# Performance work log

Hardware: AMD Instinct MI355X
Metric: run time of the kernel (lower is better)

The kernel has to match this reference:

```python
import jax, jax.numpy as jnp
import numpy as np

N_NODES = 100000
N_EDGES = 1250000
N_GRAPHS = 256
IN_DIM, HID, OUT = 7, 64, 2


def setup_inputs() -> dict:
    key = jax.random.key(0)
    ks = jax.random.split(key, 10)
    x = jax.random.normal(ks[0], (N_NODES, IN_DIM), dtype=jnp.float32)
    edge_index = jax.random.randint(ks[1], (2, N_EDGES), 0, N_NODES, dtype=jnp.int64)
    batch = jnp.sort(jax.random.randint(ks[2], (N_NODES,), 0, N_GRAPHS, dtype=jnp.int64))
    def glorot(k, shape):
        lim = float(np.sqrt(6.0 / (shape[0] + shape[1])))
        return jax.random.uniform(k, shape, jnp.float32, -lim, lim)
    return {
        "x": x, "edge_index": edge_index, "batch": batch,
        "W1": glorot(ks[3], (IN_DIM, HID)), "b1": jnp.zeros((HID,), jnp.float32),
        "W2": glorot(ks[4], (HID, HID)),   "b2": jnp.zeros((HID,), jnp.float32),
        "W3": glorot(ks[5], (HID, HID)),   "b3": jnp.zeros((HID,), jnp.float32),
        "Wl": glorot(ks[6], (HID, OUT)),   "bl": jnp.zeros((OUT,), jnp.float32),
    }


def _gcn_conv(x, src, dst, W, b, n_nodes):
    # PyG GCNConv: add self-loops, symmetric deg^{-1/2} normalization,
    # linear transform, scatter-add aggregation at target nodes, + bias.
    deg = jax.ops.segment_sum(jnp.ones_like(dst, dtype=x.dtype), dst, num_segments=n_nodes)
    dinv = jnp.where(deg > 0, jax.lax.rsqrt(deg), 0.0)
    norm = dinv[src] * dinv[dst]                      # [E+N]
    h = x @ W                                         # [N, out]
    msg = h[src] * norm[:, None]                      # gather + scale
    out = jax.ops.segment_sum(msg, dst, num_segments=n_nodes)
    return out + b


def reference(x, edge_index, batch, W1, b1, W2, b2, W3, b3, Wl, bl):
    n = x.shape[0]
    loop = jnp.arange(n, dtype=edge_index.dtype)
    src = jnp.concatenate([edge_index[0], loop])      # self-loops appended once
    dst = jnp.concatenate([edge_index[1], loop])

    h = jax.nn.relu(_gcn_conv(x, src, dst, W1, b1, n))
    h = jax.nn.relu(_gcn_conv(h, src, dst, W2, b2, n))
    h = _gcn_conv(h, src, dst, W3, b3, n)

    # global_mean_pool over graphs
    sums = jax.ops.segment_sum(h, batch, num_segments=N_GRAPHS)
    cnt = jax.ops.segment_sum(jnp.ones((n,), h.dtype), batch, num_segments=N_GRAPHS)
    pooled = sums / jnp.maximum(cnt, 1.0)[:, None]    # [G, HID]

    # dropout is identity in eval mode
    return pooled @ Wl + bl                           # [G, 2]
```

## Files before the change

### kernel.cpp

```cpp
#include <hip/hip_runtime.h>
#include <hip/hip_fp16.h>

#define HID 64
#define NGRAPHS 256
#define CHUNK 4096
#define BKTSZ 512
#define BKTSH 9
#define PSH 17
#define PMASK 0x1FFFF

typedef _Float16 half8 __attribute__((ext_vector_type(8)));
typedef float f32x4 __attribute__((ext_vector_type(4)));



__global__ __launch_bounds__(256) void k_hist(
        const int* __restrict__ dst, const float* __restrict__ W2,
        const float* __restrict__ W3, const float* __restrict__ Wl,
        __half* __restrict__ Wf2, float* __restrict__ W3l,
        int* __restrict__ H, float* __restrict__ gsum,
        int e, int nbkt, int nchunk) {
    __shared__ int cnt4[4][256];
    const int t = threadIdx.x, b = blockIdx.x;
    const int gtid = b * 256 + t;
    if (gtid < 512) {
        int p = gtid;
        int kt = p >> 8, c = (p >> 6) & 3, lane = p & 63;
        int quad = lane >> 4, m = lane & 15;
#pragma unroll
        for (int j = 0; j < 8; ++j) {
            int k = kt * 32 + quad * 8 + j;
            int ch = c * 16 + m;
            Wf2[(size_t)p * 8 + j] = __float2half(W2[k * HID + ch]);
        }
    }
    if (b == 0) {
        for (int i = t; i < NGRAPHS * 2; i += 256) gsum[i] = 0.0f;
        if (t < 128) {
            int j = t >> 1, o = t & 1;
            float s = 0.0f;
#pragma unroll
            for (int k = 0; k < HID; ++k) s += W3[j * HID + k] * Wl[k * 2 + o];
            W3l[j * 2 + o] = s;
        }
    }
    for (int i = t; i < 1024; i += 256) ((int*)cnt4)[i] = 0;
    __syncthreads();
    const int w = t >> 6;
#pragma unroll
    for (int it = 0; it < CHUNK / 1024; ++it) {
        int idx = b * CHUNK + it * 1024 + t * 4;
        if (idx + 3 < e) {
            int4 d = *(const int4*)(dst + idx);
            atomicAdd(&cnt4[w][d.x >> BKTSH], 1);
            atomicAdd(&cnt4[w][d.y >> BKTSH], 1);
            atomicAdd(&cnt4[w][d.z >> BKTSH], 1);
            atomicAdd(&cnt4[w][d.w >> BKTSH], 1);
        } else {
            for (int i = idx; i < e && i < idx + 4; ++i)
                atomicAdd(&cnt4[w][dst[i] >> BKTSH], 1);
        }
    }
    __syncthreads();
    for (int i = t; i < nbkt; i += 256)
        H[i * nchunk + b] = cnt4[0][i] + cnt4[1][i] + cnt4[2][i] + cnt4[3][i];
}


__global__ __launch_bounds__(256) void k_scan(const int* __restrict__ in,
                                              int* __restrict__ outp,
                                              int* __restrict__ bsum, int n) {
    __shared__ int sh[256];
    const int t = threadIdx.x;
    const int base = blockIdx.x * 1024 + t * 4;
    int v[4];
    int s = 0;
#pragma unroll
    for (int k = 0; k < 4; k++) {
        int i = base + k;
        v[k] = (i < n) ? in[i] : 0;
        s += v[k];
    }
    sh[t] = s;
    __syncthreads();
#pragma unroll
    for (int off = 1; off < 256; off <<= 1) {
        int add = (t >= off) ? sh[t - off] : 0;
        __syncthreads();
        sh[t] += add;
        __syncthreads();
    }
    int run = sh[t] - s;
#pragma unroll
    for (int k = 0; k < 4; k++) {
        int i = base + k;
        if (i < n) outp[i] = run;
        run += v[k];
    }
    if (t == 255) bsum[blockIdx.x] = sh[255];
}


__global__ __launch_bounds__(256) void k_scatter(
        const int* __restrict__ src, const int* __restrict__ dst,
        const int* __restrict__ Hs, const int* __restrict__ bsum,
        int* __restrict__ packed, int e, int nbkt, int nchunk, int nscan) {
    __shared__ int off[256];
    __shared__ int lc[256];
    __shared__ int bscan[64];
    const int t = threadIdx.x, b = blockIdx.x;
    if (t < 64) bscan[t] = (t < nscan) ? bsum[t] : 0;
    __syncthreads();
#pragma unroll
    for (int o = 1; o < 64; o <<= 1) {
        int add = (t < 64 && t >= o) ? bscan[t - o] : 0;
        __syncthreads();
        if (t < 64) bscan[t] += add;
        __syncthreads();
    }
    for (int i = t; i < nbkt; i += 256) {
        int idx = i * nchunk + b;
        int q = idx >> 10;
        off[i] = Hs[idx] + (q ? bscan[q - 1] : 0);
        lc[i] = 0;
    }
    __syncthreads();
#pragma unroll
    for (int it = 0; it < CHUNK / 1024; ++it) {
        int idx = b * CHUNK + it * 1024 + t * 4;
        if (idx + 3 < e) {
            int4 d = *(const int4*)(dst + idx);
            int4 s = *(const int4*)(src + idx);
            int b0 = d.x >> BKTSH, b1 = d.y >> BKTSH;
            int b2 = d.z >> BKTSH, b3 = d.w >> BKTSH;
            int r0 = atomicAdd(&lc[b0], 1);
            int r1 = atomicAdd(&lc[b1], 1);
            int r2 = atomicAdd(&lc[b2], 1);
            int r3 = atomicAdd(&lc[b3], 1);
            packed[off[b0] + r0] = s.x | ((d.x & (BKTSZ - 1)) << PSH);
            packed[off[b1] + r1] = s.y | ((d.y & (BKTSZ - 1)) << PSH);
            packed[off[b2] + r2] = s.z | ((d.z & (BKTSZ - 1)) << PSH);
            packed[off[b3] + r3] = s.w | ((d.w & (BKTSZ - 1)) << PSH);
        } else {
            for (int i = idx; i < e && i < idx + 4; ++i) {
                int dd = dst[i];
                int bk = dd >> BKTSH;
                int r = atomicAdd(&lc[bk], 1);
                packed[off[bk] + r] = src[i] | ((dd & (BKTSZ - 1)) << PSH);
            }
        }
    }
}


__global__ __launch_bounds__(256) void k_csr_build(
        const int* __restrict__ packed, const int* __restrict__ Hs,
        const int* __restrict__ bsum, int* __restrict__ rowptr,
        float* __restrict__ dinv, int* __restrict__ csr,
        const float* __restrict__ x, float* __restrict__ xt,
        int e, int n, int nbkt, int nchunk, int nscan) {
    __shared__ int cnt[BKTSZ];
    __shared__ int pref[BKTSZ];
    __shared__ int ssum[256];
    __shared__ int cnt2[BKTSZ];
    __shared__ int bscan[64];
    const int t = threadIdx.x, bkt = blockIdx.x;
    if (t < 64) bscan[t] = (t < nscan) ? bsum[t] : 0;
    if (bkt == 0 && t == 0) rowptr[n] = e;
    cnt[t] = 0; cnt[t + 256] = 0;
    cnt2[t] = 0; cnt2[t + 256] = 0;
    __syncthreads();
#pragma unroll
    for (int o = 1; o < 64; o <<= 1) {
        int add = (t < 64 && t >= o) ? bscan[t - o] : 0;
        __syncthreads();
        if (t < 64) bscan[t] += add;
        __syncthreads();
    }
    int i0 = bkt * nchunk;
    int q0 = i0 >> 10;
    int segStart = Hs[i0] + (q0 ? bscan[q0 - 1] : 0);
    int segEnd = e;
    if (bkt + 1 < nbkt) {
        int i1 = (bkt + 1) * nchunk;
        int q1 = i1 >> 10;
        segEnd = Hs[i1] + (q1 ? bscan[q1 - 1] : 0);
    }
    for (int j = segStart + t; j < segEnd; j += 256)
        atomicAdd(&cnt[(packed[j] >> PSH) & (BKTSZ - 1)], 1);
    __syncthreads();
    int a0 = cnt[2 * t], a1 = cnt[2 * t + 1];
    int s = a0 + a1;
    ssum[t] = s;
    __syncthreads();
#pragma unroll
    for (int off = 1; off < 256; off <<= 1) {
        int add = (t >= off) ? ssum[t - off] : 0;
        __syncthreads();
        ssum[t] += add;
        __syncthreads();
    }
    int p = ssum[t] - s;
    pref[2 * t] = p;
    pref[2 * t + 1] = p + a0;
    __syncthreads();
    for (int i = t; i < BKTSZ; i += 256) {
        int node = bkt * BKTSZ + i;
        if (node < n) {
            rowptr[node] = segStart + pref[i];
            dinv[node] = rsqrtf((float)(cnt[i] + 1));
        }
    }
    for (int j = segStart + t; j < segEnd; j += 256) {
        int pk = packed[j];
        int ld = (pk >> PSH) & (BKTSZ - 1);
        int r = atomicAdd(&cnt2[ld], 1);
        csr[segStart + pref[ld] + r] = pk & PMASK;
    }
    for (int i = t; i < BKTSZ * 8; i += 256) {
        int nl = i >> 3, k = i & 7;
        int node = bkt * BKTSZ + nl;
        if (node < n)
            xt[(size_t)node * 8 + k] =
                (k < 7) ? x[(size_t)node * 7 + k] * rsqrtf((float)(cnt[nl] + 1))
                        : 0.0f;
    }
}

__device__ __forceinline__ void add_h8(float* a, int4 raw) {
    const __half2* p = (const __half2*)&raw;
#pragma unroll
    for (int i = 0; i < 4; ++i) {
        float2 f = __half22float2(p[i]);
        a[2 * i] += f.x;
        a[2 * i + 1] += f.y;
    }
}


__global__ __launch_bounds__(256) void k_aggx_gemm(
        const int* __restrict__ rowptr, const int* __restrict__ csr,
        const float* __restrict__ xt, const float* __restrict__ b,
        const float* __restrict__ dinv, const float* __restrict__ W1,
        const __half* __restrict__ Wf, __half* __restrict__ hout,
        int n_nodes) {
    __shared__ __half act[16 * 72];
    __shared__ float W1s[7 * HID];
    const int t = threadIdx.x;
    const int n0 = blockIdx.x * 16;
    const int nl = t >> 4;
    const int node = n0 + nl;
    const int l16 = t & 15;
    const float4* xt4 = (const float4*)xt;
    const float4* b4 = (const float4*)b;

    for (int i = t; i < 7 * HID; i += 256) W1s[i] = W1[i];

    float acc8[8];
#pragma unroll
    for (int i = 0; i < 8; ++i) acc8[i] = 0.0f;

    float4 av = make_float4(0.0f, 0.0f, 0.0f, 0.0f);
    float dv = 0.0f;
    if (node < n_nodes) {
        int beg = rowptr[node], end = rowptr[node + 1];
        dv = dinv[node];
        if (l16 == 0) {
            float4 s0 = xt4[(size_t)node * 2];
            float4 s1 = xt4[(size_t)node * 2 + 1];
            acc8[0] += s0.x; acc8[1] += s0.y; acc8[2] += s0.z; acc8[3] += s0.w;
            acc8[4] += s1.x; acc8[5] += s1.y; acc8[6] += s1.z; acc8[7] += s1.w;
        }
        int j = beg;
        for (; j + 15 < end; j += 16) {
            int e = csr[j + l16];
            float4 r0 = xt4[(size_t)e * 2];
            float4 r1 = xt4[(size_t)e * 2 + 1];
            acc8[0] += r0.x; acc8[1] += r0.y; acc8[2] += r0.z; acc8[3] += r0.w;
            acc8[4] += r1.x; acc8[5] += r1.y; acc8[6] += r1.z; acc8[7] += r1.w;
        }
        int rem = end - j;
        if (l16 < rem) {
            int e = csr[j + l16];
            float4 r0 = xt4[(size_t)e * 2];
            float4 r1 = xt4[(size_t)e * 2 + 1];
            acc8[0] += r0.x; acc8[1] += r0.y; acc8[2] += r0.z; acc8[3] += r0.w;
            acc8[4] += r1.x; acc8[5] += r1.y; acc8[6] += r1.z; acc8[7] += r1.w;
        }
    }
#pragma unroll
    for (int o = 8; o; o >>= 1)
#pragma unroll
        for (int i = 0; i < 7; ++i)
            acc8[i] += __shfl_xor(acc8[i], o, 16);

    if (node < n_nodes) {
        float4 bb = b4[l16];
#pragma unroll
        for (int i = 0; i < 4; ++i) {
            int c = l16 * 4 + i;
            float dot = 0.0f;
#pragma unroll
            for (int k = 0; k < 7; ++k) dot += acc8[k] * W1s[k * HID + c];
            float v = ((const float*)&bb)[i] + dv * dot;
            ((float*)&av)[i] = fmaxf(v, 0.0f);
        }
    }
    {
        __half2 p0 = __floats2half2_rn(av.x, av.y);
        __half2 p1 = __floats2half2_rn(av.z, av.w);
        int2 pk;
        pk.x = *(int*)&p0;
        pk.y = *(int*)&p1;
        *(int2*)&act[nl * 72 + l16 * 4] = pk;
    }
    __syncthreads();

    const int wave = t >> 6, lane = t & 63;
    const int quad = lane >> 4, m = lane & 15;
    const half8* Wf8 = (const half8*)Wf;
    f32x4 acc = {0.0f, 0.0f, 0.0f, 0.0f};
#pragma unroll
    for (int kt = 0; kt < 2; ++kt) {
        half8 a = *(const half8*)&act[m * 72 + kt * 32 + quad * 8];
        half8 bv = Wf8[(kt * 4 + wave) * 64 + lane];
        acc = __builtin_amdgcn_mfma_f32_16x16x32_f16(a, bv, acc, 0, 0, 0);
    }
#pragma unroll
    for (int r = 0; r < 4; ++r) {
        int nd = n0 + quad * 4 + r;
        if (nd < n_nodes)
            hout[(size_t)nd * HID + wave * 16 + m] =
                __float2half(acc[r] * dinv[nd]);
    }
}


__global__ __launch_bounds__(256) void k_agg_z(
        const int* __restrict__ rowptr, const int* __restrict__ csr,
        const __half* __restrict__ h, const float* __restrict__ b,
        const float* __restrict__ dinv, const float* __restrict__ W3l,
        float2* __restrict__ zbuf, int n_nodes) {
    const int t = threadIdx.x;
    const int n0 = blockIdx.x * 16;
    const int nl = t >> 4;
    const int node = n0 + nl;
    const int l16 = t & 15;
    const int cb = l16 & 7;
    const int hf = l16 >> 3;
    const int4* h16 = (const int4*)h;

    float w3l0[8], w3l1[8], bb8[8];
#pragma unroll
    for (int i = 0; i < 8; ++i) {
        w3l0[i] = W3l[(cb * 8 + i) * 2 + 0];
        w3l1[i] = W3l[(cb * 8 + i) * 2 + 1];
        bb8[i] = b[cb * 8 + i];
    }

    float acc8[8];
#pragma unroll
    for (int i = 0; i < 8; ++i) acc8[i] = 0.0f;

    float dv = 0.0f;
    if (node < n_nodes) {
        int beg = rowptr[node], end = rowptr[node + 1];
        dv = dinv[node];
        if (hf == 0)
            add_h8(acc8, h16[(size_t)node * 8 + cb]);
        int j = beg;
        for (; j + 7 < end; j += 8) {
            int e8 = csr[j + (l16 & 7)];
            int4 r[4];
#pragma unroll
            for (int q = 0; q < 4; ++q) {
                int sid = __shfl(e8, 2 * q + hf, 8);
                r[q] = h16[(size_t)sid * 8 + cb];
            }
#pragma unroll
            for (int q = 0; q < 4; ++q) add_h8(acc8, r[q]);
        }
        if (j + 3 < end) {
            int e4 = csr[j + (l16 & 3)];
            int4 r[2];
#pragma unroll
            for (int q = 0; q < 2; ++q) {
                int sid = __shfl(e4, 2 * q + hf, 4);
                r[q] = h16[(size_t)sid * 8 + cb];
            }
            add_h8(acc8, r[0]);
            add_h8(acc8, r[1]);
            j += 4;
        }
        for (; j < end; ++j)
            if (hf == 0) add_h8(acc8, h16[(size_t)csr[j] * 8 + cb]);
    }
#pragma unroll
    for (int i = 0; i < 8; ++i) acc8[i] += __shfl_xor(acc8[i], 8, 16);
    float p0 = 0.0f, p1 = 0.0f;
#pragma unroll
    for (int i = 0; i < 8; ++i) {
        float v = fmaxf(bb8[i] + dv * acc8[i], 0.0f);
        p0 += v * w3l0[i];
        p1 += v * w3l1[i];
    }
#pragma unroll
    for (int o = 4; o; o >>= 1) {
        p0 += __shfl_xor(p0, o, 16);
        p1 += __shfl_xor(p1, o, 16);
    }
    if (node < n_nodes && l16 == 0)
        zbuf[node] = make_float2(p0 * dv, p1 * dv);
}


__global__ __launch_bounds__(256) void k_zagg_part(
        const int* __restrict__ rowptr, const int* __restrict__ csr,
        const float2* __restrict__ zbuf, const float* __restrict__ dinv,
        const int* __restrict__ batch, float* __restrict__ partv,
        int* __restrict__ partg, float* __restrict__ gsum, int n_nodes) {
    __shared__ float2 ys[16];
    __shared__ int bg[16];
    const int t = threadIdx.x;
    const int n0 = blockIdx.x * 16;
    const int nl = t >> 4;
    const int node = n0 + nl;
    const int q = t & 15;

    if (t < 16) {
        int nd = n0 + t;
        bg[t] = (nd < n_nodes) ? batch[nd] : -1;
    }

    float2 yv = make_float2(0.0f, 0.0f);
    if (node < n_nodes) {
        int beg = rowptr[node], end = rowptr[node + 1];
        float2 acc = make_float2(0.0f, 0.0f);
        if (q == 0) acc = zbuf[node];
        int j = beg;
        for (; j + 15 < end; j += 16) {
            int e = csr[j + q];
            float2 v = zbuf[e];
            acc.x += v.x; acc.y += v.y;
        }
        int rem = end - j;
        if (q < rem) {
            int e = csr[j + q];
            float2 v = zbuf[e];
            acc.x += v.x; acc.y += v.y;
        }
#pragma unroll
        for (int o = 8; o; o >>= 1) {
            acc.x += __shfl_xor(acc.x, o, 16);
            acc.y += __shfl_xor(acc.y, o, 16);
        }
        float dv = dinv[node];
        yv = make_float2(acc.x * dv, acc.y * dv);
    }
    if (q == 0) ys[nl] = yv;
    __syncthreads();

    if (t == 0) {
        const int g0 = bg[0];
        const int g15 = bg[15];
        float2 s0 = make_float2(0.0f, 0.0f), s1 = make_float2(0.0f, 0.0f);
        for (int i = 0; i < 16; ++i) {
            int g = bg[i];
            float2 v = ys[i];
            if (g == g0) { s0.x += v.x; s0.y += v.y; }
            else if (g == g15) { s1.x += v.x; s1.y += v.y; }
            else if (g >= 0) {
                atomicAdd(&gsum[g * 2 + 0], v.x);
                atomicAdd(&gsum[g * 2 + 1], v.y);
            }
        }
        partv[(size_t)blockIdx.x * 4 + 0] = s0.x;
        partv[(size_t)blockIdx.x * 4 + 1] = s0.y;
        partv[(size_t)blockIdx.x * 4 + 2] = s1.x;
        partv[(size_t)blockIdx.x * 4 + 3] = s1.y;
        partg[blockIdx.x * 2 + 0] = g0;
        partg[blockIdx.x * 2 + 1] = (g15 != g0) ? g15 : -1;
    }
}


__global__ __launch_bounds__(256) void k_pool_head(
        const float* __restrict__ partv, const int* __restrict__ partg,
        const float* __restrict__ gsum, const int* __restrict__ batch,
        const float* __restrict__ b3, const float* __restrict__ Wl,
        const float* __restrict__ bl, float* __restrict__ out, int n_nodes) {
    int g = blockIdx.x;
    int lo = 0, hi = n_nodes;
    while (lo < hi) { int m = (lo + hi) >> 1; if (batch[m] < g) lo = m + 1; else hi = m; }
    int nstart = lo;
    hi = n_nodes;
    while (lo < hi) { int m = (lo + hi) >> 1; if (batch[m] < g + 1) lo = m + 1; else hi = m; }
    int nend = lo;

    const int t = threadIdx.x;
    float ax = 0.0f, ay = 0.0f;
    if (nend > nstart) {
        int b0 = nstart >> 4, b1 = (nend - 1) >> 4;
        for (int b = b0 + t; b <= b1; b += 256) {
            if (partg[b * 2 + 0] == g) { ax += partv[(size_t)b * 4 + 0]; ay += partv[(size_t)b * 4 + 1]; }
            if (partg[b * 2 + 1] == g) { ax += partv[(size_t)b * 4 + 2]; ay += partv[(size_t)b * 4 + 3]; }
        }
    }
    __shared__ float rx[256], ry[256];
    rx[t] = ax; ry[t] = ay;
    __syncthreads();
    for (int s2 = 128; s2; s2 >>= 1) {
        if (t < s2) { rx[t] += rx[t + s2]; ry[t] += ry[t + s2]; }
        __syncthreads();
    }
    if (t < 2) {
        float cntf = fmaxf((float)(nend - nstart), 1.0f);
        float s = ((t == 0) ? rx[0] : ry[0]) + gsum[g * 2 + t];
        float hb = 0.0f;
        for (int c = 0; c < HID; ++c) hb += b3[c] * Wl[c * 2 + t];
        out[g * 2 + t] = s / cntf + hb + bl[t];
    }
}


extern "C" void kernel_launch(void* const* d_in, const int* in_sizes, int n_in,
                              void* d_out, int out_size, void* d_ws, size_t ws_size,
                              hipStream_t stream) {
    const float* x     = (const float*)d_in[0];
    const int*   ei    = (const int*)d_in[1];
    const int*   batch = (const int*)d_in[2];
    const float* W1    = (const float*)d_in[3];
    const float* b1    = (const float*)d_in[4];
    const float* W2    = (const float*)d_in[5];
    const float* b2    = (const float*)d_in[6];
    const float* W3    = (const float*)d_in[7];
    const float* b3    = (const float*)d_in[8];
    const float* Wl    = (const float*)d_in[9];
    const float* bl    = (const float*)d_in[10];
    float* out = (float*)d_out;

    const int N = in_sizes[0] / 7;
    const int E = in_sizes[1] / 2;
    const int* src = ei;
    const int* dst = ei + E;

    const int nbkt   = (N + BKTSZ - 1) >> BKTSH;
    const int nchunk = (E + CHUNK - 1) / CHUNK;
    const int lenH   = nbkt * nchunk;
    const int nscan  = (lenH + 1023) / 1024;

    char* ws = (char*)d_ws;
    size_t off = 0;
    auto carve = [&](size_t bytes) {
        void* p = ws + off;
        off = (off + bytes + 255) & ~(size_t)255;
        return p;
    };
    int*    H      = (int*)carve((size_t)lenH * 4);
    int*    Hs     = (int*)carve((size_t)lenH * 4);
    int*    bsum   = (int*)carve(512 * 4);
    int*    packed = (int*)carve((size_t)E * 4);
    int*    csr    = (int*)carve((size_t)E * 4);
    int*    rowptr = (int*)carve((size_t)(N + 1) * 4);
    float*  dinv   = (float*)carve((size_t)N * 4);
    __half* Wf2    = (__half*)carve(4096 * 2);
    float*  W3l    = (float*)carve(128 * 4);
    float*  gsum   = (float*)carve((size_t)NGRAPHS * 2 * 4);
    float*  xt     = (float*)carve((size_t)(N + 64) * 8 * 4);
    __half* bufB   = (__half*)carve((size_t)(N + 64) * HID * 2);
    float2* zbuf   = (float2*)carve((size_t)(N + 64) * 8);

    const int nb_agg = (N + 15) / 16;
    float* partv = (float*)carve((size_t)nb_agg * 4 * 4);
    int*   partg = (int*)carve((size_t)nb_agg * 2 * 4);

    k_hist<<<nchunk, 256, 0, stream>>>(dst, W2, W3, Wl, Wf2, W3l, H, gsum,
                                       E, nbkt, nchunk);
    k_scan<<<nscan, 256, 0, stream>>>(H, Hs, bsum, lenH);
    k_scatter<<<nchunk, 256, 0, stream>>>(src, dst, Hs, bsum, packed,
                                          E, nbkt, nchunk, nscan);
    k_csr_build<<<nbkt, 256, 0, stream>>>(packed, Hs, bsum, rowptr, dinv, csr,
                                          x, xt, E, N, nbkt, nchunk, nscan);

    k_aggx_gemm<<<nb_agg, 256, 0, stream>>>(rowptr, csr, xt, b1, dinv, W1,
                                            Wf2, bufB, N);
    k_agg_z<<<nb_agg, 256, 0, stream>>>(rowptr, csr, bufB, b2, dinv, W3l,
                                        zbuf, N);
    k_zagg_part<<<nb_agg, 256, 0, stream>>>(rowptr, csr, zbuf, dinv, batch,
                                            partv, partg, gsum, N);

    k_pool_head<<<NGRAPHS, 256, 0, stream>>>(partv, partg, gsum, batch,
                                             b3, Wl, bl, out, N);
}
```

Before: 195.2 us.

## Replace two-pass bucket sort CSR build with global atomic degree count and scatter

Replaces the bucketed histogram, scan, packed scatter and per-bucket CSR build with a direct per-node degree count using global atomics, a per-block scan that also computes dinv and pre-scaled features, and a scatter that places each edge using a global atomic cursor per destination. This removes the packed intermediate buffer, one pass over the edges and one kernel launch. In exchange it relies on heavily contended global atomics on random addresses and gives a nondeterministic neighbor order within each row, which can change floating-point summation order and locality in later aggregation.

```diff
diff --git a/kernel.cpp b/kernel.cpp
--- a/kernel.cpp
+++ b/kernel.cpp
@@ -3,24 +3,17 @@
 
 #define HID 64
 #define NGRAPHS 256
-#define CHUNK 4096
-#define BKTSZ 512
-#define BKTSH 9
-#define PSH 17
-#define PMASK 0x1FFFF
 
 typedef _Float16 half8 __attribute__((ext_vector_type(8)));
 typedef float f32x4 __attribute__((ext_vector_type(4)));
 
 
 
-__global__ __launch_bounds__(256) void k_hist(
+__global__ __launch_bounds__(256) void k_deg(
         const int* __restrict__ dst, const float* __restrict__ W2,
         const float* __restrict__ W3, const float* __restrict__ Wl,
         __half* __restrict__ Wf2, float* __restrict__ W3l,
-        int* __restrict__ H, float* __restrict__ gsum,
-        int e, int nbkt, int nchunk) {
-    __shared__ int cnt4[4][256];
+        int* __restrict__ deg, float* __restrict__ gsum, int e) {
     const int t = threadIdx.x, b = blockIdx.x;
     const int gtid = b * 256 + t;
     if (gtid < 512) {
@@ -44,186 +37,112 @@
             W3l[j * 2 + o] = s;
         }
     }
-    for (int i = t; i < 1024; i += 256) ((int*)cnt4)[i] = 0;
-    __syncthreads();
-    const int w = t >> 6;
-#pragma unroll
-    for (int it = 0; it < CHUNK / 1024; ++it) {
-        int idx = b * CHUNK + it * 1024 + t * 4;
-        if (idx + 3 < e) {
-            int4 d = *(const int4*)(dst + idx);
-            atomicAdd(&cnt4[w][d.x >> BKTSH], 1);
-            atomicAdd(&cnt4[w][d.y >> BKTSH], 1);
-            atomicAdd(&cnt4[w][d.z >> BKTSH], 1);
-            atomicAdd(&cnt4[w][d.w >> BKTSH], 1);
-        } else {
-            for (int i = idx; i < e && i < idx + 4; ++i)
-                atomicAdd(&cnt4[w][dst[i] >> BKTSH], 1);
-        }
-    }
-    __syncthreads();
-    for (int i = t; i < nbkt; i += 256)
-        H[i * nchunk + b] = cnt4[0][i] + cnt4[1][i] + cnt4[2][i] + cnt4[3][i];
-}
-
-
-__global__ __launch_bounds__(256) void k_scan(const int* __restrict__ in,
-                                              int* __restrict__ outp,
-                                              int* __restrict__ bsum, int n) {
+    int idx = b * 1024 + t * 4;
+    if (idx + 3 < e) {
+        int4 d = *(const int4*)(dst + idx);
+        atomicAdd(&deg[d.x], 1);
+        atomicAdd(&deg[d.y], 1);
+        atomicAdd(&deg[d.z], 1);
+        atomicAdd(&deg[d.w], 1);
+    } else {
+        for (int i = idx; i < e && i < idx + 4; ++i)
+            atomicAdd(&deg[dst[i]], 1);
+    }
+}
+
+
+__global__ __launch_bounds__(256) void k_scan2(
+        const int* __restrict__ deg, const float* __restrict__ x,
+        int* __restrict__ rowptr, int* __restrict__ wpcnt,
+        int* __restrict__ bsum, float* __restrict__ dinv,
+        float* __restrict__ xt, int n) {
     __shared__ int sh[256];
-    const int t = threadIdx.x;
-    const int base = blockIdx.x * 1024 + t * 4;
-    int v[4];
-    int s = 0;
-#pragma unroll
-    for (int k = 0; k < 4; k++) {
-        int i = base + k;
-        v[k] = (i < n) ? in[i] : 0;
-        s += v[k];
-    }
+    __shared__ int degS[512];
+    const int t = threadIdx.x, b = blockIdx.x;
+    const int base = b * 512;
+    const int i0 = base + 2 * t, i1 = i0 + 1;
+    int v0 = (i0 < n) ? deg[i0] : 0;
+    int v1 = (i1 < n) ? deg[i1] : 0;
+    degS[2 * t] = v0;
+    degS[2 * t + 1] = v1;
+    int s = v0 + v1;
     sh[t] = s;
     __syncthreads();
 #pragma unroll
-    for (int off = 1; off < 256; off <<= 1) {
-        int add = (t >= off) ? sh[t - off] : 0;
+    for (int o = 1; o < 256; o <<= 1) {
+        int add = (t >= o) ? sh[t - o] : 0;
         __syncthreads();
         sh[t] += add;
         __syncthreads();
     }
     int run = sh[t] - s;
-#pragma unroll
-    for (int k = 0; k < 4; k++) {
-        int i = base + k;
-        if (i < n) outp[i] = run;
-        run += v[k];
-    }
-    if (t == 255) bsum[blockIdx.x] = sh[255];
-}
-
-
-__global__ __launch_bounds__(256) void k_scatter(
-        const int* __restrict__ src, const int* __restrict__ dst,
-        const int* __restrict__ Hs, const int* __restrict__ bsum,
-        int* __restrict__ packed, int e, int nbkt, int nchunk, int nscan) {
-    __shared__ int off[256];
-    __shared__ int lc[256];
-    __shared__ int bscan[64];
-    const int t = threadIdx.x, b = blockIdx.x;
-    if (t < 64) bscan[t] = (t < nscan) ? bsum[t] : 0;
+    if (i0 < n) {
+        rowptr[i0] = run;  wpcnt[i0] = run;
+        dinv[i0] = rsqrtf((float)(v0 + 1));
+    }
+    if (i1 < n) {
+        rowptr[i1] = run + v0;  wpcnt[i1] = run + v0;
+        dinv[i1] = rsqrtf((float)(v1 + 1));
+    }
+    if (t == 255) bsum[b] = sh[255];
     __syncthreads();
-#pragma unroll
-    for (int o = 1; o < 64; o <<= 1) {
-        int add = (t < 64 && t >= o) ? bscan[t - o] : 0;
-        __syncthreads();
-        if (t < 64) bscan[t] += add;
-        __syncthreads();
-    }
-    for (int i = t; i < nbkt; i += 256) {
-        int idx = i * nchunk + b;
-        int q = idx >> 10;
-        off[i] = Hs[idx] + (q ? bscan[q - 1] : 0);
-        lc[i] = 0;
-    }
-    __syncthreads();
-#pragma unroll
-    for (int it = 0; it < CHUNK / 1024; ++it) {
-        int idx = b * CHUNK + it * 1024 + t * 4;
-        if (idx + 3 < e) {
-            int4 d = *(const int4*)(dst + idx);
-            int4 s = *(const int4*)(src + idx);
-            int b0 = d.x >> BKTSH, b1 = d.y >> BKTSH;
-            int b2 = d.z >> BKTSH, b3 = d.w >> BKTSH;
-            int r0 = atomicAdd(&lc[b0], 1);
-            int r1 = atomicAdd(&lc[b1], 1);
-            int r2 = atomicAdd(&lc[b2], 1);
-            int r3 = atomicAdd(&lc[b3], 1);
-            packed[off[b0] + r0] = s.x | ((d.x & (BKTSZ - 1)) << PSH);
-            packed[off[b1] + r1] = s.y | ((d.y & (BKTSZ - 1)) << PSH);
-            packed[off[b2] + r2] = s.z | ((d.z & (BKTSZ - 1)) << PSH);
-            packed[off[b3] + r3] = s.w | ((d.w & (BKTSZ - 1)) << PSH);
-        } else {
-            for (int i = idx; i < e && i < idx + 4; ++i) {
-                int dd = dst[i];
-                int bk = dd >> BKTSH;
-                int r = atomicAdd(&lc[bk], 1);
-                packed[off[bk] + r] = src[i] | ((dd & (BKTSZ - 1)) << PSH);
-            }
-        }
-    }
-}
-
-
-__global__ __launch_bounds__(256) void k_csr_build(
-        const int* __restrict__ packed, const int* __restrict__ Hs,
-        const int* __restrict__ bsum, int* __restrict__ rowptr,
-        float* __restrict__ dinv, int* __restrict__ csr,
-        const float* __restrict__ x, float* __restrict__ xt,
-        int e, int n, int nbkt, int nchunk, int nscan) {
-    __shared__ int cnt[BKTSZ];
-    __shared__ int pref[BKTSZ];
-    __shared__ int ssum[256];
-    __shared__ int cnt2[BKTSZ];
-    __shared__ int bscan[64];
-    const int t = threadIdx.x, bkt = blockIdx.x;
-    if (t < 64) bscan[t] = (t < nscan) ? bsum[t] : 0;
-    if (bkt == 0 && t == 0) rowptr[n] = e;
-    cnt[t] = 0; cnt[t + 256] = 0;
-    cnt2[t] = 0; cnt2[t + 256] = 0;
-    __syncthreads();
-#pragma unroll
-    for (int o = 1; o < 64; o <<= 1) {
-        int add = (t < 64 && t >= o) ? bscan[t - o] : 0;
-        __syncthreads();
-        if (t < 64) bscan[t] += add;
-        __syncthreads();
-    }
-    int i0 = bkt * nchunk;
-    int q0 = i0 >> 10;
-    int segStart = Hs[i0] + (q0 ? bscan[q0 - 1] : 0);
-    int segEnd = e;
-    if (bkt + 1 < nbkt) {
-        int i1 = (bkt + 1) * nchunk;
-        int q1 = i1 >> 10;
-        segEnd = Hs[i1] + (q1 ? bscan[q1 - 1] : 0);
-    }
-    for (int j = segStart + t; j < segEnd; j += 256)
-        atomicAdd(&cnt[(packed[j] >> PSH) & (BKTSZ - 1)], 1);
-    __syncthreads();
-    int a0 = cnt[2 * t], a1 = cnt[2 * t + 1];
-    int s = a0 + a1;
-    ssum[t] = s;
-    __syncthreads();
-#pragma unroll
-    for (int off = 1; off < 256; off <<= 1) {
-        int add = (t >= off) ? ssum[t - off] : 0;
-        __syncthreads();
-        ssum[t] += add;
-        __syncthreads();
-    }
-    int p = ssum[t] - s;
-    pref[2 * t] = p;
-    pref[2 * t + 1] = p + a0;
-    __syncthreads();
-    for (int i = t; i < BKTSZ; i += 256) {
-        int node = bkt * BKTSZ + i;
-        if (node < n) {
-            rowptr[node] = segStart + pref[i];
-            dinv[node] = rsqrtf((float)(cnt[i] + 1));
-        }
-    }
-    for (int j = segStart + t; j < segEnd; j += 256) {
-        int pk = packed[j];
-        int ld = (pk >> PSH) & (BKTSZ - 1);
-        int r = atomicAdd(&cnt2[ld], 1);
-        csr[segStart + pref[ld] + r] = pk & PMASK;
-    }
-    for (int i = t; i < BKTSZ * 8; i += 256) {
+    for (int i = t; i < 512 * 8; i += 256) {
         int nl = i >> 3, k = i & 7;
-        int node = bkt * BKTSZ + nl;
+        int node = base + nl;
         if (node < n)
             xt[(size_t)node * 8 + k] =
-                (k < 7) ? x[(size_t)node * 7 + k] * rsqrtf((float)(cnt[nl] + 1))
+                (k < 7) ? x[(size_t)node * 7 + k] * rsqrtf((float)(degS[nl] + 1))
                         : 0.0f;
+    }
+}
+
+
+__global__ __launch_bounds__(256) void k_scatter2(
+        const int* __restrict__ src, const int* __restrict__ dst,
+        int* __restrict__ rowptr, const int* __restrict__ bsum,
+        int* __restrict__ wpcnt, int* __restrict__ csr,
+        int e, int n, int nscan) {
+    __shared__ int bscan[256];
+    const int t = threadIdx.x, b = blockIdx.x;
+    bscan[t] = (t < nscan) ? bsum[t] : 0;
+    __syncthreads();
+#pragma unroll
+    for (int o = 1; o < 256; o <<= 1) {
+        int add = (t >= o) ? bscan[t - o] : 0;
+        __syncthreads();
+        bscan[t] += add;
+        __syncthreads();
+    }
+    for (int i = b * 256 + t; i < n; i += gridDim.x * 256) {
+        int q = i >> 9;
+        rowptr[i] += (q ? bscan[q - 1] : 0);
+    }
+    if (b == 0 && t == 0) rowptr[n] = e;
+    int idx = b * 1024 + t * 4;
+    if (idx + 3 < e) {
+        int4 d = *(const int4*)(dst + idx);
+        int4 s = *(const int4*)(src + idx);
+        int q0 = d.x >> 9, q1 = d.y >> 9, q2 = d.z >> 9, q3 = d.w >> 9;
+        int o0 = q0 ? bscan[q0 - 1] : 0;
+        int o1 = q1 ? bscan[q1 - 1] : 0;
+        int o2 = q2 ? bscan[q2 - 1] : 0;
+        int o3 = q3 ? bscan[q3 - 1] : 0;
+        int p0 = atomicAdd(&wpcnt[d.x], 1);
+        int p1 = atomicAdd(&wpcnt[d.y], 1);
+        int p2 = atomicAdd(&wpcnt[d.z], 1);
+        int p3 = atomicAdd(&wpcnt[d.w], 1);
+        csr[p0 + o0] = s.x;
+        csr[p1 + o1] = s.y;
+        csr[p2 + o2] = s.z;
+        csr[p3 + o3] = s.w;
+    } else {
+        for (int i = idx; i < e && i < idx + 4; ++i) {
+            int dd = dst[i];
+            int q = dd >> 9;
+            int o = q ? bscan[q - 1] : 0;
+            int p = atomicAdd(&wpcnt[dd], 1);
+            csr[p + o] = src[i];
+        }
     }
 }
 
@@ -544,10 +463,8 @@
     const int* src = ei;
     const int* dst = ei + E;
 
-    const int nbkt   = (N + BKTSZ - 1) >> BKTSH;
-    const int nchunk = (E + CHUNK - 1) / CHUNK;
-    const int lenH   = nbkt * nchunk;
-    const int nscan  = (lenH + 1023) / 1024;
+    const int nscan = (N + 511) >> 9;
+    const int nb_e  = (E + 1023) / 1024;
 
     char* ws = (char*)d_ws;
     size_t off = 0;
@@ -556,12 +473,11 @@
         off = (off + bytes + 255) & ~(size_t)255;
         return p;
     };
-    int*    H      = (int*)carve((size_t)lenH * 4);
-    int*    Hs     = (int*)carve((size_t)lenH * 4);
-    int*    bsum   = (int*)carve(512 * 4);
-    int*    packed = (int*)carve((size_t)E * 4);
+    int*    deg    = (int*)carve((size_t)N * 4);
+    int*    wpcnt  = (int*)carve((size_t)N * 4);
+    int*    rowptr = (int*)carve((size_t)(N + 1) * 4);
+    int*    bsum   = (int*)carve(256 * 4);
     int*    csr    = (int*)carve((size_t)E * 4);
-    int*    rowptr = (int*)carve((size_t)(N + 1) * 4);
     float*  dinv   = (float*)carve((size_t)N * 4);
     __half* Wf2    = (__half*)carve(4096 * 2);
     float*  W3l    = (float*)carve(128 * 4);
@@ -574,13 +490,12 @@
     float* partv = (float*)carve((size_t)nb_agg * 4 * 4);
     int*   partg = (int*)carve((size_t)nb_agg * 2 * 4);
 
-    k_hist<<<nchunk, 256, 0, stream>>>(dst, W2, W3, Wl, Wf2, W3l, H, gsum,
-                                       E, nbkt, nchunk);
-    k_scan<<<nscan, 256, 0, stream>>>(H, Hs, bsum, lenH);
-    k_scatter<<<nchunk, 256, 0, stream>>>(src, dst, Hs, bsum, packed,
-                                          E, nbkt, nchunk, nscan);
-    k_csr_build<<<nbkt, 256, 0, stream>>>(packed, Hs, bsum, rowptr, dinv, csr,
-                                          x, xt, E, N, nbkt, nchunk, nscan);
+    hipMemsetAsync(deg, 0, (size_t)N * 4, stream);
+    k_deg<<<nb_e, 256, 0, stream>>>(dst, W2, W3, Wl, Wf2, W3l, deg, gsum, E);
+    k_scan2<<<nscan, 256, 0, stream>>>(deg, x, rowptr, wpcnt, bsum, dinv,
+                                       xt, N);
+    k_scatter2<<<nb_e, 256, 0, stream>>>(src, dst, rowptr, bsum, wpcnt, csr,
+                                         E, N, nscan);
 
     k_aggx_gemm<<<nb_agg, 256, 0, stream>>>(rowptr, csr, xt, b1, dinv, W1,
                                             Wf2, bufB, N);
```

Measured after the change: 315.1 us. 61.4% more time.
